# Kernel tuning notes

Measured on AMD Instinct MI355X. Metric: run time of the kernel, lower is better.

Reference implementation:

```python
import jax, jax.numpy as jnp
import numpy as np

B, T, D = 4, 4096, 512

def setup_inputs() -> dict:
    key = jax.random.key(0)
    k1, k2, k3 = jax.random.split(key, 3)
    z_hat = jax.random.normal(k1, (B, T, D), dtype=jnp.float32)
    P = jax.random.uniform(k2, (B, T), dtype=jnp.float32)
    lengths = jax.random.randint(k3, (B,), 0, T).astype(jnp.int32)
    return {"z_hat": z_hat, "P": P, "lengths": lengths}

def reference(z_hat, P, lengths):
    # z_hat: [B, T, D], P: [B, T], lengths: [B]
    Bs, Tc, _ = z_hat.shape
    P_clamped = jnp.clip(P, 0.0, 1.0 - 1e-6)
    q = 1.0 - P_clamped
    # inclusive cumulative sum of log q (same as padded-cumsum[:,1:] in torch)
    log_cumprod_q = jnp.cumsum(jnp.log(q), axis=1)                 # [B, T]
    log_P = jnp.log(jnp.clip(P_clamped, 1e-6, None))               # [B, T]
    # log_M[b, t, k] = log P[b, k] + logcum[b, t] - logcum[b, k], causal (k <= t)
    log_M = (log_P[:, None, :]
             + log_cumprod_q[:, :, None]
             - log_cumprod_q[:, None, :])                          # [B, T, T]
    t_idx = jnp.arange(Tc)
    causal = t_idx[:, None] >= t_idx[None, :]                      # k <= t kept
    M = jnp.where(causal[None, :, :], jnp.exp(log_M), 0.0)         # [B, T, T]
    z_bar = jnp.einsum('btk,bkd->btd', M, z_hat)                   # [B, T, D]
    padding_mask = t_idx[None, :] < lengths[:, None]               # [B, T]
    return z_bar * padding_mask[:, :, None].astype(z_bar.dtype)
```

## Files before the change

### kernel.cpp

```cpp
#include <hip/hip_runtime.h>


#define CHUNK 64
#define MAX_NC 512

__global__ __launch_bounds__(512) void k_local(
    const float* __restrict__ z, const float* __restrict__ P,
    float* __restrict__ S, float* __restrict__ A,
    int B, int T, int D, int NC) {
  int blk = blockIdx.x;
  int b = blk / NC, c = blk % NC;
  int t0 = c * CHUNK;
  __shared__ float p_s[CHUNK], q_s[CHUNK];
  int tid = threadIdx.x;
  if (tid < CHUNK) {
    int tg = t0 + tid;
    float p = (tg < T) ? P[(size_t)b * T + tg] : 0.0f;
    p = fminf(fmaxf(p, 0.0f), 1.0f - 1e-6f);
    q_s[tid] = 1.0f - p;
    p_s[tid] = fmaxf(p, 1e-6f);
  }
  __syncthreads();
  int nt = min(CHUNK, T - t0);
  for (int d = tid; d < D; d += blockDim.x) {
    const float* zp = z + ((size_t)b * T + t0) * D + d;
    float s = 0.0f, r = 1.0f;
    for (int t = 0; t < nt; ++t) {
      s = fmaf(q_s[t], s, p_s[t] * zp[(size_t)t * D]);
      r *= q_s[t];
    }
    S[((size_t)b * NC + c) * D + d] = s;
    if (d == 0) A[b * NC + c] = r;
  }
}

__global__ __launch_bounds__(512) void k_apply(
    const float* __restrict__ z, const float* __restrict__ P,
    const float* __restrict__ S, const float* __restrict__ A,
    const int* __restrict__ lengths, float* __restrict__ out,
    int B, int T, int D, int NC) {
  int blk = blockIdx.x;
  int b = blk / NC, c = blk % NC;
  int t0 = c * CHUNK;
  __shared__ float p_s[CHUNK], q_s[CHUNK];
  __shared__ float a_s[MAX_NC];
  int tid = threadIdx.x;
  if (tid < CHUNK) {
    int tg = t0 + tid;
    float p = (tg < T) ? P[(size_t)b * T + tg] : 0.0f;
    p = fminf(fmaxf(p, 0.0f), 1.0f - 1e-6f);
    q_s[tid] = 1.0f - p;
    p_s[tid] = fmaxf(p, 1e-6f);
  }
  for (int i = tid; i < NC; i += blockDim.x) a_s[i] = A[b * NC + i];
  __syncthreads();
  int L = lengths[b];
  int nt = min(CHUNK, T - t0);
  for (int d = tid; d < D; d += blockDim.x) {
    float carry = 0.0f, w = 1.0f;
    for (int cp = c - 1; cp >= 0; --cp) {
      carry = fmaf(S[((size_t)b * NC + cp) * D + d], w, carry);
      w *= a_s[cp];
    }
    const float* zp = z + ((size_t)b * T + t0) * D + d;
    float* op = out + ((size_t)b * T + t0) * D + d;
    float s = carry;
    for (int t = 0; t < nt; ++t) {
      s = fmaf(q_s[t], s, p_s[t] * zp[(size_t)t * D]);
      op[(size_t)t * D] = ((t0 + t) < L) ? s : 0.0f;
    }
  }
}

extern "C" void kernel_launch(void* const* d_in, const int* in_sizes, int n_in,
                              void* d_out, int out_size, void* d_ws, size_t ws_size,
                              hipStream_t stream) {
  const float* z = (const float*)d_in[0];
  const float* P = (const float*)d_in[1];
  const int* lengths = (const int*)d_in[2];
  float* out = (float*)d_out;

  int B = in_sizes[2];
  int T = in_sizes[1] / B;
  int D = in_sizes[0] / in_sizes[1];
  int NC = (T + CHUNK - 1) / CHUNK;

  float* S = (float*)d_ws;
  float* A = S + (size_t)B * NC * D;

  dim3 grid(B * NC), block(512);
  k_local<<<grid, block, 0, stream>>>(z, P, S, A, B, T, D, NC);
  k_apply<<<grid, block, 0, stream>>>(z, P, S, A, lengths, out, B, T, D, NC);
}
```

Baseline: 97.49 us.

## Replace quadratic carry loop with parallel chunk scan, float4 access and length skipping

Replaces the per-chunk serial accumulation over all previous chunk summaries with a dedicated Hillis-Steele scan kernel that computes every chunk's carry in parallel. The chunk size shrinks and block size drops to raise block count, and z/out accesses are vectorized as float4. Chunks beyond each sequence's length skip reading z and only write zeros. Adds a third kernel launch and a carry workspace buffer, and assumes D divisible by 4 and NC no larger than the block-size limit.

```diff
diff --git a/kernel.cpp b/kernel.cpp
--- a/kernel.cpp
+++ b/kernel.cpp
@@ -1,18 +1,28 @@
 #include <hip/hip_runtime.h>
 
 
-#define CHUNK 64
-#define MAX_NC 512
+#define CHUNK 16
+#define NCMAX 512
 
-__global__ __launch_bounds__(512) void k_local(
+__global__ __launch_bounds__(128) void k_local(
     const float* __restrict__ z, const float* __restrict__ P,
+    const int* __restrict__ lengths,
     float* __restrict__ S, float* __restrict__ A,
     int B, int T, int D, int NC) {
   int blk = blockIdx.x;
   int b = blk / NC, c = blk % NC;
   int t0 = c * CHUNK;
+  int tid = threadIdx.x;
+  int D4 = D >> 2;
+  float4* S4 = (float4*)(S + ((size_t)b * NC + c) * D);
+  int L = lengths[b];
+  if (t0 >= L) {
+    float4 zero = make_float4(0.f, 0.f, 0.f, 0.f);
+    for (int d4 = tid; d4 < D4; d4 += blockDim.x) S4[d4] = zero;
+    if (tid == 0) A[b * NC + c] = 1.0f;
+    return;
+  }
   __shared__ float p_s[CHUNK], q_s[CHUNK];
-  int tid = threadIdx.x;
   if (tid < CHUNK) {
     int tg = t0 + tid;
     float p = (tg < T) ? P[(size_t)b * T + tg] : 0.0f;
@@ -22,29 +32,87 @@
   }
   __syncthreads();
   int nt = min(CHUNK, T - t0);
-  for (int d = tid; d < D; d += blockDim.x) {
-    const float* zp = z + ((size_t)b * T + t0) * D + d;
-    float s = 0.0f, r = 1.0f;
-    for (int t = 0; t < nt; ++t) {
-      s = fmaf(q_s[t], s, p_s[t] * zp[(size_t)t * D]);
-      r *= q_s[t];
+  const float4* z4 = (const float4*)(z + ((size_t)b * T + t0) * D);
+  for (int d4 = tid; d4 < D4; d4 += blockDim.x) {
+    float4 s = make_float4(0.f, 0.f, 0.f, 0.f);
+#pragma unroll
+    for (int t = 0; t < CHUNK; ++t) {
+      if (t < nt) {
+        float4 zv = z4[(size_t)t * D4 + d4];
+        float q = q_s[t], pe = p_s[t];
+        s.x = fmaf(q, s.x, pe * zv.x);
+        s.y = fmaf(q, s.y, pe * zv.y);
+        s.z = fmaf(q, s.z, pe * zv.z);
+        s.w = fmaf(q, s.w, pe * zv.w);
+      }
     }
-    S[((size_t)b * NC + c) * D + d] = s;
-    if (d == 0) A[b * NC + c] = r;
+    S4[d4] = s;
+  }
+  if (tid == 0) {
+    float r = 1.0f;
+    for (int t = 0; t < nt; ++t) r *= q_s[t];
+    A[b * NC + c] = r;
   }
 }
 
-__global__ __launch_bounds__(512) void k_apply(
+__global__ void k_carry(
+    const float* __restrict__ S, const float* __restrict__ A,
+    float* __restrict__ Carry, int D4, int NC) {
+  int b = blockIdx.x / D4;
+  int d4 = blockIdx.x % D4;
+  int c = threadIdx.x;
+  __shared__ float sh_a[NCMAX];
+  __shared__ float4 sh_v[NCMAX];
+  float a = A[b * NC + c];
+  const float4* S4 = (const float4*)S;
+  float4 sv = S4[((size_t)b * NC + c) * D4 + d4];
+  sh_a[c] = a;
+  sh_v[c] = sv;
+  __syncthreads();
+  for (int off = 1; off < NC; off <<= 1) {
+    float ap = 1.0f;
+    float4 vp = make_float4(0.f, 0.f, 0.f, 0.f);
+    bool has = (c >= off);
+    if (has) { ap = sh_a[c - off]; vp = sh_v[c - off]; }
+    __syncthreads();
+    if (has) {
+      sv.x = fmaf(a, vp.x, sv.x);
+      sv.y = fmaf(a, vp.y, sv.y);
+      sv.z = fmaf(a, vp.z, sv.z);
+      sv.w = fmaf(a, vp.w, sv.w);
+      a *= ap;
+      sh_a[c] = a;
+      sh_v[c] = sv;
+    }
+    __syncthreads();
+  }
+  float4 car = make_float4(0.f, 0.f, 0.f, 0.f);
+  if (c > 0) car = sh_v[c - 1];
+  float4* C4 = (float4*)Carry;
+  C4[((size_t)b * NC + c) * D4 + d4] = car;
+}
+
+__global__ __launch_bounds__(128) void k_apply(
     const float* __restrict__ z, const float* __restrict__ P,
-    const float* __restrict__ S, const float* __restrict__ A,
-    const int* __restrict__ lengths, float* __restrict__ out,
+    const float* __restrict__ Carry, const int* __restrict__ lengths,
+    float* __restrict__ out,
     int B, int T, int D, int NC) {
   int blk = blockIdx.x;
   int b = blk / NC, c = blk % NC;
   int t0 = c * CHUNK;
+  int tid = threadIdx.x;
+  int D4 = D >> 2;
+  int nt = min(CHUNK, T - t0);
+  float4* o4 = (float4*)(out + ((size_t)b * T + t0) * D);
+  int L = lengths[b];
+  if (t0 >= L) {
+    float4 zero = make_float4(0.f, 0.f, 0.f, 0.f);
+    for (int t = 0; t < nt; ++t)
+      for (int d4 = tid; d4 < D4; d4 += blockDim.x)
+        o4[(size_t)t * D4 + d4] = zero;
+    return;
+  }
   __shared__ float p_s[CHUNK], q_s[CHUNK];
-  __shared__ float a_s[MAX_NC];
-  int tid = threadIdx.x;
   if (tid < CHUNK) {
     int tg = t0 + tid;
     float p = (tg < T) ? P[(size_t)b * T + tg] : 0.0f;
@@ -52,22 +120,23 @@
     q_s[tid] = 1.0f - p;
     p_s[tid] = fmaxf(p, 1e-6f);
   }
-  for (int i = tid; i < NC; i += blockDim.x) a_s[i] = A[b * NC + i];
   __syncthreads();
-  int L = lengths[b];
-  int nt = min(CHUNK, T - t0);
-  for (int d = tid; d < D; d += blockDim.x) {
-    float carry = 0.0f, w = 1.0f;
-    for (int cp = c - 1; cp >= 0; --cp) {
-      carry = fmaf(S[((size_t)b * NC + cp) * D + d], w, carry);
-      w *= a_s[cp];
-    }
-    const float* zp = z + ((size_t)b * T + t0) * D + d;
-    float* op = out + ((size_t)b * T + t0) * D + d;
-    float s = carry;
-    for (int t = 0; t < nt; ++t) {
-      s = fmaf(q_s[t], s, p_s[t] * zp[(size_t)t * D]);
-      op[(size_t)t * D] = ((t0 + t) < L) ? s : 0.0f;
+  const float4* z4 = (const float4*)(z + ((size_t)b * T + t0) * D);
+  const float4* C4 = (const float4*)(Carry + ((size_t)b * NC + c) * D);
+  for (int d4 = tid; d4 < D4; d4 += blockDim.x) {
+    float4 s = C4[d4];
+#pragma unroll
+    for (int t = 0; t < CHUNK; ++t) {
+      if (t < nt) {
+        float4 zv = z4[(size_t)t * D4 + d4];
+        float q = q_s[t], pe = p_s[t];
+        s.x = fmaf(q, s.x, pe * zv.x);
+        s.y = fmaf(q, s.y, pe * zv.y);
+        s.z = fmaf(q, s.z, pe * zv.z);
+        s.w = fmaf(q, s.w, pe * zv.w);
+        float4 o = ((t0 + t) < L) ? s : make_float4(0.f, 0.f, 0.f, 0.f);
+        o4[(size_t)t * D4 + d4] = o;
+      }
     }
   }
 }
@@ -84,11 +153,13 @@
   int T = in_sizes[1] / B;
   int D = in_sizes[0] / in_sizes[1];
   int NC = (T + CHUNK - 1) / CHUNK;
+  int D4 = D >> 2;
 
   float* S = (float*)d_ws;
   float* A = S + (size_t)B * NC * D;
+  float* Carry = A + (((size_t)B * NC + 3) & ~(size_t)3);
 
-  dim3 grid(B * NC), block(512);
-  k_local<<<grid, block, 0, stream>>>(z, P, S, A, B, T, D, NC);
-  k_apply<<<grid, block, 0, stream>>>(z, P, S, A, lengths, out, B, T, D, NC);
+  k_local<<<dim3(B * NC), dim3(128), 0, stream>>>(z, P, lengths, S, A, B, T, D, NC);
+  k_carry<<<dim3(B * D4), dim3(NC), 0, stream>>>(S, A, Carry, D4, NC);
+  k_apply<<<dim3(B * NC), dim3(128), 0, stream>>>(z, P, Carry, lengths, out, B, T, D, NC);
 }
```

Result: slower. 105.1 us (+7.8%).
